# Kernel tuning notes

Measured on AMD Instinct MI355X. Metric: run time of the kernel, lower is better.

## Reference

```python
import jax, jax.numpy as jnp
import numpy as np

B, D_DATA, D_DICT0, N_SAE, D_DICT = 2048, 768, 128, 128, 32


def _kaiming_uniform(key, shape, fan_in):
    # torch.nn.init.kaiming_uniform_ default: bound = sqrt(6 / fan_in) / sqrt(5-gain stuff) ~ use gain=sqrt(2)? match torch default a=sqrt(5) not needed; plain kaiming_uniform_ uses gain=sqrt(2): bound = sqrt(6/fan_in)*? Keep simple: bound = sqrt(6.0/fan_in)
    bound = np.sqrt(6.0 / fan_in)
    return jax.random.uniform(key, shape, jnp.float32, -bound, bound)


def setup_inputs() -> dict:
    key = jax.random.key(0)
    ks = jax.random.split(key, 6)
    x = jax.random.normal(ks[0], (B, D_DATA), jnp.float32)
    # top-level SAE params
    W_enc0 = _kaiming_uniform(ks[1], (D_DATA, D_DICT0), D_DATA)
    b_enc0 = jnp.zeros((D_DICT0,), jnp.float32)
    W_dec0 = _kaiming_uniform(ks[2], (D_DICT0, D_DATA), D_DICT0)
    W_dec0 = W_dec0 / jnp.linalg.norm(W_dec0, axis=-1, keepdims=True)
    b_dec0 = jnp.zeros((D_DATA,), jnp.float32)
    # sublayer (hierarchical) per-expert params
    W_enc1 = _kaiming_uniform(ks[3], (N_SAE, D_DATA, D_DICT), D_DATA)
    b_enc1 = jnp.zeros((N_SAE, D_DICT), jnp.float32)
    W_dec1 = _kaiming_uniform(ks[4], (N_SAE, D_DICT, D_DATA), D_DICT)
    W_dec1 = W_dec1 / jnp.linalg.norm(W_dec1, axis=-1, keepdims=True)
    b_dec1 = jnp.zeros((N_SAE, D_DATA), jnp.float32)
    return {"x": x, "W_enc0": W_enc0, "b_enc0": b_enc0, "W_dec0": W_dec0,
            "b_dec0": b_dec0, "W_enc1": W_enc1, "b_enc1": b_enc1,
            "W_dec1": W_dec1, "b_dec1": b_dec1}


def reference(x, W_enc0, b_enc0, W_dec0, b_dec0, W_enc1, b_enc1, W_dec1, b_dec1):
    # ---- sae_0 (standard SAE; scale/unscale are identity) ----
    acts0 = jax.nn.relu((x - b_dec0) @ W_enc0 + b_enc0)        # [B, D_DICT0]
    x0 = acts0 @ W_dec0 + b_dec0                               # [B, D_DATA]
    # ---- binary gate over experts (n_sae == d_dict0) ----
    gate = (acts0 > 0).astype(x.dtype)                         # [B, N_SAE]
    # ---- sublayer: gather-encode-decode-scatter, expressed densely with a
    # binary mask (gate only selects membership; gate value is not multiplied).
    # Avoid materializing [B, N_SAE, D_DATA] by distributing (x - b_dec1[j]):
    pre = (jnp.einsum('bd,jdk->bjk', x, W_enc1)
           - jnp.einsum('jd,jdk->jk', b_dec1, W_enc1)[None]
           + b_enc1[None])                                     # [B, N_SAE, D_DICT]
    acts1 = jax.nn.relu(pre) * gate[:, :, None]                # zero out ungated
    # scatter_add over experts: sum_j gated (acts1[b,j] @ W_dec1[j] + b_dec1[j])
    dec = jnp.einsum('bjk,jkd->bd', acts1, W_dec1) + gate @ b_dec1  # [B, D_DATA]
    return x0 + dec
```

## Files before the change

### kernel.cpp

```cpp
#include <hip/hip_runtime.h>
#include <hip/hip_bf16.h>
#include <stdint.h>

#define B_SZ   2048
#define DDATA  768
#define NSAE   128
#define NJK    4096
#define KA2    4352
#define SPLITK 4
#define KC2    1088

typedef unsigned short u16;
typedef short bf16x8 __attribute__((ext_vector_type(8)));
typedef float f32x4  __attribute__((ext_vector_type(4)));

static __device__ __forceinline__ u16 f2bf(float f) {
  __hip_bfloat16 h = __float2bfloat16(f);
  return *reinterpret_cast<u16*>(&h);
}

static __device__ __forceinline__ void gload16(const u16* g, u16* l) {
  __builtin_amdgcn_global_load_lds(
      (const __attribute__((address_space(1))) unsigned int*)g,
      (__attribute__((address_space(3))) unsigned int*)l,
      16, 0, 0);
}

__global__ __launch_bounds__(256) void k_front(const float* __restrict__ x,
                                               const float* __restrict__ We0,
                                               const float* __restrict__ be0,
                                               const float* __restrict__ bd0,
                                               const float* __restrict__ We1,
                                               const float* __restrict__ bd1,
                                               const float* __restrict__ be1,
                                               const float* __restrict__ Wd1,
                                               const float* __restrict__ Wd0,
                                               u16* __restrict__ W1T,
                                               float* __restrict__ cvp,
                                               u16* __restrict__ B2T,
                                               u16* __restrict__ xb,
                                               u16* __restrict__ A2) {
  __shared__ float smem[6280];
  const int bid = blockIdx.x, t = threadIdx.x;
  if (bid < 256) {
    const int b0 = bid * 8;
    float* xs  = smem;
    float* xns = smem + 6144;
    float* wns = smem + 6152;
#pragma unroll
    for (int i = 0; i < 6; ++i) {
      int idx = t + i * 256;
      int r = idx / 192, c4 = idx % 192;
      size_t go = (size_t)(b0 + r) * DDATA + c4 * 4;
      float4 v = *(const float4*)&x[go];
      ushort4 o;
      o.x = f2bf(v.x); o.y = f2bf(v.y); o.z = f2bf(v.z); o.w = f2bf(v.w);
      *(ushort4*)&xb[go] = o;
      float4 b4 = *(const float4*)&bd0[c4 * 4];
      v.x -= b4.x; v.y -= b4.y; v.z -= b4.z; v.w -= b4.w;
      *(float4*)&xs[r * DDATA + c4 * 4] = v;
    }
    __syncthreads();
    const int ln = t & 63, rg = t >> 6;
#pragma unroll
    for (int rr = 0; rr < 2; ++rr) {
      int r = rg * 2 + rr;
      float a = 0.f;
#pragma unroll
      for (int q = 0; q < 12; ++q) { float xv = xs[r * DDATA + ln + q * 64]; a += xv * xv; }
#pragma unroll
      for (int sh = 32; sh; sh >>= 1) a += __shfl_xor(a, sh, 64);
      if (ln == 0) xns[r] = a;
    }
    const int j0 = ln * 2;
    const float* xr0 = xs + (rg * 2) * DDATA;
    const float* xr1 = xr0 + DDATA;
    float pa0 = be0[j0], pa1 = be0[j0 + 1];
    float pb0 = pa0, pb1 = pa1;
    float wq0 = 0.f, wq1 = 0.f;
#define GBODY(WQ)                                                         \
    for (int d = 0; d < DDATA; d += 4) {                                  \
      _Pragma("unroll")                                                   \
      for (int dd = 0; dd < 4; ++dd) {                                    \
        float2 w2 = *(const float2*)&We0[(size_t)(d + dd) * 128 + j0];    \
        float a0 = xr0[d + dd], a1 = xr1[d + dd];                         \
        pa0 += a0 * w2.x; pa1 += a0 * w2.y;                               \
        pb0 += a1 * w2.x; pb1 += a1 * w2.y;                               \
        if (WQ) { wq0 += w2.x * w2.x; wq1 += w2.y * w2.y; }               \
      }                                                                   \
    }
    if (rg == 0) { GBODY(1); wns[j0] = sqrtf(wq0); wns[j0 + 1] = sqrtf(wq1); }
    else         { GBODY(0); }
#undef GBODY
    __syncthreads();
    const float sA = sqrtf(xns[rg * 2]), sB = sqrtf(xns[rg * 2 + 1]);
    const float w0 = wns[j0], w1 = wns[j0 + 1];
    const size_t rowA = (size_t)(b0 + rg * 2) * KA2;
    const size_t rowB = rowA + KA2;
    unsigned pka = (unsigned)f2bf(pa0 > 0.f ? pa0 : 0.f) |
                   ((unsigned)f2bf(pa1 > 0.f ? pa1 : 0.f) << 16);
    unsigned gka = (pa0 > 0.f ? 0x3F80u : 0u) | (pa1 > 0.f ? 0x3F800000u : 0u);
    unsigned pkb = (unsigned)f2bf(pb0 > 0.f ? pb0 : 0.f) |
                   ((unsigned)f2bf(pb1 > 0.f ? pb1 : 0.f) << 16);
    unsigned gkb = (pb0 > 0.f ? 0x3F80u : 0u) | (pb1 > 0.f ? 0x3F800000u : 0u);
    *(unsigned*)&A2[rowA + NJK + j0]       = pka;
    *(unsigned*)&A2[rowA + NJK + 128 + j0] = gka;
    *(unsigned*)&A2[rowB + NJK + j0]       = pkb;
    *(unsigned*)&A2[rowB + NJK + 128 + j0] = gkb;
    const float tA0 = 1e-4f * sA * w0, tA1 = 1e-4f * sA * w1;
    const float tB0 = 1e-4f * sB * w0, tB1 = 1e-4f * sB * w1;
#pragma unroll
    for (int c = 0; c < 4; ++c) {
      float pv = c == 0 ? pa0 : c == 1 ? pa1 : c == 2 ? pb0 : pb1;
      float tv = c == 0 ? tA0 : c == 1 ? tA1 : c == 2 ? tB0 : tB1;
      unsigned long long mask = __ballot(fabsf(pv) <= tv);
      const int bb = b0 + rg * 2 + (c >> 1);
      while (mask) {
        int src = (int)__builtin_ctzll(mask);
        mask &= mask - 1;
        int jj = src * 2 + (c & 1);
        double acc = 0.0;
#pragma unroll
        for (int q = 0; q < 12; ++q) {
          int d = ln + q * 64;
          acc += (double)(x[(size_t)bb * DDATA + d] - bd0[d]) *
                 (double)We0[(size_t)d * 128 + jj];
        }
#pragma unroll
        for (int sh = 32; sh; sh >>= 1) acc += __shfl_xor(acc, sh, 64);
        if (ln == src) {
          double pd = acc + (double)be0[jj];
          size_t rw = (size_t)bb * KA2;
          A2[rw + NJK + jj]       = f2bf(pd > 0.0 ? (float)pd : 0.f);
          A2[rw + NJK + 128 + jj] = (pd > 0.0) ? (u16)0x3F80 : (u16)0;
        }
      }
    }
  } else if (bid < 640) {
    const int e = bid - 256;
    const int j = e & 127, seg = e >> 7;
    float* ts  = smem;
    float* bds = smem + 64 * 33;
    float* red = smem + 64 * 33 + 64;
    const int k = t & 31, g = t >> 5;
    float cacc = 0.f;
    for (int db = seg * 4; db < seg * 4 + 4; ++db) {
      const float* src = We1 + (size_t)j * 24576 + db * 2048;
#pragma unroll
      for (int i = 0; i < 8; ++i) {
        int ee = t + i * 256;
        ts[(ee >> 5) * 33 + (ee & 31)] = src[ee];
      }
      if (t < 64) bds[t] = bd1[(size_t)j * DDATA + db * 64 + t];
      __syncthreads();
#pragma unroll
      for (int i = 0; i < 8; ++i) {
        int ee = t + i * 256;
        int kk = ee >> 6, d = ee & 63;
        W1T[(size_t)(j * 32 + kk) * DDATA + db * 64 + d] = f2bf(ts[d * 33 + kk]);
      }
#pragma unroll
      for (int q = 0; q < 8; ++q) {
        int d = g + 8 * q;
        cacc += ts[d * 33 + k] * bds[d];
      }
      __syncthreads();
    }
    red[g * 32 + k] = cacc;
    __syncthreads();
    if (g == 0) {
      float s = 0.f;
#pragma unroll
      for (int q = 0; q < 8; ++q) s += red[q * 32 + k];
      cvp[seg * 4096 + j * 32 + k] = (seg == 0 ? be1[j * 32 + k] : 0.f) - s;
    }
  } else {
    const int e2 = bid - 640;
    const int rb = e2 / 12, dbk = e2 % 12;
    const float* src; int r0, base;
    if (rb < 64)      { src = Wd1; r0 = rb * 64;        base = 0;    }
    else if (rb < 66) { src = Wd0; r0 = (rb - 64) * 64; base = 4096; }
    else              { src = bd1; r0 = (rb - 66) * 64; base = 4224; }
    const int d0 = dbk * 64;
#pragma unroll
    for (int i = 0; i < 16; ++i) {
      int ee = t + i * 256;
      int ri = ee >> 6, di = ee & 63;
      smem[ri * 65 + di] = src[(size_t)(r0 + ri) * DDATA + d0 + di];
    }
    __syncthreads();
#pragma unroll
    for (int i = 0; i < 16; ++i) {
      int ee = t + i * 256;
      int di = ee >> 6, ri = ee & 63;
      B2T[(size_t)(d0 + di) * KA2 + base + r0 + ri] = f2bf(smem[ri * 65 + di]);
    }
  }
}

template<int BM, int BN, int EPI>
__global__ __launch_bounds__(256) void k_gemm(const u16* __restrict__ A,
                                              const u16* __restrict__ Bm,
                                              int K, int Kc,
                                              float* __restrict__ outF,
                                              u16* __restrict__ A2,
                                              const float* __restrict__ cvec) {
  constexpr int WM = BM / 32, WN = BN / 32;
  __shared__ __align__(16) u16 As[BM * 64];
  __shared__ __align__(16) u16 Bs[BN * 64];
  __shared__ u16 gate_s[BM * 4];
  __shared__ float cv_s[BN];
  const int tid = threadIdx.x;
  int bx, by, bz;
  {
    const int h = blockIdx.x;
    if (EPI == 1) {
      const int l = (h & 7) * 64 + (h >> 3);
      const int g2 = l >> 6, w = l & 63;
      by = w >> 2; bx = (g2 << 2) + (w & 3); bz = 0;
    } else {
      const int l = (h & 7) * 96 + (h >> 3);
      bx = l >> 7; const int r2 = l & 127; bz = r2 >> 5; by = r2 & 31;
    }
  }
  const int kbase = bz * Kc;
  const u16* Ab = A  + (size_t)(by * BM) * K;
  const u16* Bb = Bm + (size_t)(bx * BN) * K;
  const int wave = tid >> 6, lane = tid & 63;
  const int wr = wave >> 1, wc = wave & 1;
  const int m0 = wr * (BM / 2), n0 = wc * (BN / 2);
  const int lm = lane & 15, qd = lane >> 4;

  if (EPI == 1) {
    for (int e = tid; e < BM * 4; e += 256) {
      int r = e >> 2, q = e & 3;
      gate_s[e] = A2[(size_t)(by * BM + r) * KA2 + NJK + 128 + bx * 4 + q];
    }
    for (int e = tid; e < BN; e += 256)
      cv_s[e] = cvec[bx * BN + e] + cvec[4096 + bx * BN + e] + cvec[8192 + bx * BN + e];
  }

  f32x4 acc[WM][WN];
  const f32x4 zero = {0.f, 0.f, 0.f, 0.f};
  for (int mi = 0; mi < WM; ++mi)
    for (int ni = 0; ni < WN; ++ni) acc[mi][ni] = zero;

  for (int k0 = kbase; k0 < kbase + Kc; k0 += 64) {
#pragma unroll
    for (int i = 0; i < BM / 32; ++i) {
      int id = tid + 256 * i;
      int row = id >> 3, u = id & 7;
      gload16(Ab + (size_t)row * K + k0 + ((u ^ (row & 7)) * 8), &As[id * 8]);
    }
#pragma unroll
    for (int i = 0; i < BN / 32; ++i) {
      int id = tid + 256 * i;
      int row = id >> 3, u = id & 7;
      gload16(Bb + (size_t)row * K + k0 + ((u ^ (row & 7)) * 8), &Bs[id * 8]);
    }
    __syncthreads();
#pragma unroll
    for (int s = 0; s < 2; ++s) {
      const int swz = ((s << 2) + qd) ^ (lm & 7);
      bf16x8 af[WM], bfv[WN];
#pragma unroll
      for (int mi = 0; mi < WM; ++mi)
        af[mi] = *(const bf16x8*)&As[(m0 + mi * 16 + lm) * 64 + swz * 8];
#pragma unroll
      for (int ni = 0; ni < WN; ++ni)
        bfv[ni] = *(const bf16x8*)&Bs[(n0 + ni * 16 + lm) * 64 + swz * 8];
#pragma unroll
      for (int mi = 0; mi < WM; ++mi)
#pragma unroll
        for (int ni = 0; ni < WN; ++ni)
          acc[mi][ni] = __builtin_amdgcn_mfma_f32_16x16x32_bf16(af[mi], bfv[ni],
                                                                acc[mi][ni], 0, 0, 0);
    }
    __syncthreads();
  }

  const int rb = qd * 4;
#pragma unroll
  for (int mi = 0; mi < WM; ++mi) {
#pragma unroll
    for (int ni = 0; ni < WN; ++ni) {
#pragma unroll
      for (int r = 0; r < 4; ++r) {
        int ml = m0 + mi * 16 + rb + r;
        int nl = n0 + ni * 16 + lm;
        int gm = by * BM + ml;
        int gn = bx * BN + nl;
        float v = acc[mi][ni][r];
        if (EPI == 1) {
          v += cv_s[nl];
          v = v > 0.f ? v : 0.f;
          u16 gbit = gate_s[ml * 4 + (nl >> 5)];
          v = gbit ? v : 0.f;
          float vn = __shfl_xor(v, 1, 64);
          if ((lm & 1) == 0) {
            unsigned pk = (unsigned)f2bf(v) | ((unsigned)f2bf(vn) << 16);
            *(unsigned*)&A2[(size_t)gm * KA2 + gn] = pk;
          }
        } else {
          outF[((size_t)bz * B_SZ + gm) * DDATA + gn] = v;
        }
      }
    }
  }
}

__global__ __launch_bounds__(256) void k_reduce(const float* __restrict__ part,
                                                const float* __restrict__ bias,
                                                float* __restrict__ out) {
  const int N4 = B_SZ * DDATA / 4;
  int i = blockIdx.x * 256 + threadIdx.x;
  const float4* p4 = (const float4*)part;
  float4 s = p4[i];
#pragma unroll
  for (int z = 1; z < SPLITK; ++z) {
    float4 t = p4[i + z * N4];
    s.x += t.x; s.y += t.y; s.z += t.z; s.w += t.w;
  }
  float4 b = ((const float4*)bias)[i % (DDATA / 4)];
  s.x += b.x; s.y += b.y; s.z += b.z; s.w += b.w;
  ((float4*)out)[i] = s;
}

extern "C" void kernel_launch(void* const* d_in, const int* in_sizes, int n_in,
                              void* d_out, int out_size, void* d_ws, size_t ws_size,
                              hipStream_t stream) {
  const float* x   = (const float*)d_in[0];
  const float* We0 = (const float*)d_in[1];
  const float* be0 = (const float*)d_in[2];
  const float* Wd0 = (const float*)d_in[3];
  const float* bd0 = (const float*)d_in[4];
  const float* We1 = (const float*)d_in[5];
  const float* be1 = (const float*)d_in[6];
  const float* Wd1 = (const float*)d_in[7];
  const float* bd1 = (const float*)d_in[8];
  float* out = (float*)d_out;

  uint8_t* ws = (uint8_t*)d_ws;
  size_t off = 0;
  auto carve = [&](size_t bytes) {
    uint8_t* p = ws + off;
    off += (bytes + 255) & ~(size_t)255;
    return p;
  };
  u16*    A2   = (u16*)carve((size_t)B_SZ * KA2 * 2);
  u16*    xb   = (u16*)carve((size_t)B_SZ * DDATA * 2);
  u16*    W1T  = (u16*)carve((size_t)NJK * DDATA * 2);
  u16*    B2T  = (u16*)carve((size_t)DDATA * KA2 * 2);
  float*  cvp  = (float*)carve((size_t)3 * NJK * 4);
  float*  part = (float*)carve((size_t)SPLITK * B_SZ * DDATA * 4);

  k_front <<<1456, 256, 0, stream>>>(x, We0, be0, bd0, We1, bd1, be1, Wd1, Wd0,
                                     W1T, cvp, B2T, xb, A2);
  k_gemm<128, 128, 1><<<512, 256, 0, stream>>>(xb, W1T, DDATA, DDATA,
                                               nullptr, A2, cvp);
  k_gemm<64, 128, 2><<<768, 256, 0, stream>>>(A2, B2T, KA2, KC2,
                                              part, nullptr, nullptr);
  k_reduce<<<1536, 256, 0, stream>>>(part, bd0, out);
}
```

Baseline: 184.2 us.

## Split gate GEMV over d, move B2T transpose into encoder GEMM launch

New measurement: 163.7 us. 1.12x faster.

```diff
diff --git a/kernel.cpp b/kernel.cpp
--- a/kernel.cpp
+++ b/kernel.cpp
@@ -9,6 +9,7 @@
 #define KA2    4352
 #define SPLITK 4
 #define KC2    1088
+#define B2TB   816
 
 typedef unsigned short u16;
 typedef short bf16x8 __attribute__((ext_vector_type(8)));
@@ -33,20 +34,18 @@
                                                const float* __restrict__ We1,
                                                const float* __restrict__ bd1,
                                                const float* __restrict__ be1,
-                                               const float* __restrict__ Wd1,
-                                               const float* __restrict__ Wd0,
                                                u16* __restrict__ W1T,
                                                float* __restrict__ cvp,
-                                               u16* __restrict__ B2T,
                                                u16* __restrict__ xb,
                                                u16* __restrict__ A2) {
-  __shared__ float smem[6280];
+  __shared__ float smem[10760];
   const int bid = blockIdx.x, t = threadIdx.x;
   if (bid < 256) {
     const int b0 = bid * 8;
-    float* xs  = smem;
-    float* xns = smem + 6144;
-    float* wns = smem + 6152;
+    float* xs   = smem;
+    float* part = smem + 6144;
+    float* wqp  = smem + 10240;
+    float* xns  = smem + 10752;
 #pragma unroll
     for (int i = 0; i < 6; ++i) {
       int idx = t + i * 256;
@@ -61,10 +60,10 @@
       *(float4*)&xs[r * DDATA + c4 * 4] = v;
     }
     __syncthreads();
-    const int ln = t & 63, rg = t >> 6;
+    const int ln = t & 63, w = t >> 6;
 #pragma unroll
     for (int rr = 0; rr < 2; ++rr) {
-      int r = rg * 2 + rr;
+      int r = w * 2 + rr;
       float a = 0.f;
 #pragma unroll
       for (int q = 0; q < 12; ++q) { float xv = xs[r * DDATA + ln + q * 64]; a += xv * xv; }
@@ -73,29 +72,46 @@
       if (ln == 0) xns[r] = a;
     }
     const int j0 = ln * 2;
-    const float* xr0 = xs + (rg * 2) * DDATA;
-    const float* xr1 = xr0 + DDATA;
+    float a0[8], a1[8];
+    float wq0 = 0.f, wq1 = 0.f;
+#pragma unroll
+    for (int r = 0; r < 8; ++r) { a0[r] = 0.f; a1[r] = 0.f; }
+    const int dbase = w * 192;
+    for (int d = dbase; d < dbase + 192; d += 4) {
+      float4 xv[8];
+#pragma unroll
+      for (int r = 0; r < 8; ++r) xv[r] = *(const float4*)&xs[r * DDATA + d];
+#pragma unroll
+      for (int dd = 0; dd < 4; ++dd) {
+        float2 w2 = *(const float2*)&We0[(size_t)(d + dd) * 128 + j0];
+#pragma unroll
+        for (int r = 0; r < 8; ++r) {
+          float xr = ((const float*)&xv[r])[dd];
+          a0[r] += xr * w2.x; a1[r] += xr * w2.y;
+        }
+        wq0 += w2.x * w2.x; wq1 += w2.y * w2.y;
+      }
+    }
+#pragma unroll
+    for (int r = 0; r < 8; ++r)
+      *(float2*)&part[(w * 8 + r) * 128 + j0] = make_float2(a0[r], a1[r]);
+    *(float2*)&wqp[w * 128 + j0] = make_float2(wq0, wq1);
+    __syncthreads();
     float pa0 = be0[j0], pa1 = be0[j0 + 1];
     float pb0 = pa0, pb1 = pa1;
-    float wq0 = 0.f, wq1 = 0.f;
-#define GBODY(WQ)                                                         \
-    for (int d = 0; d < DDATA; d += 4) {                                  \
-      _Pragma("unroll")                                                   \
-      for (int dd = 0; dd < 4; ++dd) {                                    \
-        float2 w2 = *(const float2*)&We0[(size_t)(d + dd) * 128 + j0];    \
-        float a0 = xr0[d + dd], a1 = xr1[d + dd];                         \
-        pa0 += a0 * w2.x; pa1 += a0 * w2.y;                               \
-        pb0 += a1 * w2.x; pb1 += a1 * w2.y;                               \
-        if (WQ) { wq0 += w2.x * w2.x; wq1 += w2.y * w2.y; }               \
-      }                                                                   \
-    }
-    if (rg == 0) { GBODY(1); wns[j0] = sqrtf(wq0); wns[j0 + 1] = sqrtf(wq1); }
-    else         { GBODY(0); }
-#undef GBODY
-    __syncthreads();
-    const float sA = sqrtf(xns[rg * 2]), sB = sqrtf(xns[rg * 2 + 1]);
-    const float w0 = wns[j0], w1 = wns[j0 + 1];
-    const size_t rowA = (size_t)(b0 + rg * 2) * KA2;
+    float wn0 = 0.f, wn1 = 0.f;
+#pragma unroll
+    for (int q = 0; q < 4; ++q) {
+      float2 prA = *(const float2*)&part[(q * 8 + 2 * w) * 128 + j0];
+      float2 prB = *(const float2*)&part[(q * 8 + 2 * w + 1) * 128 + j0];
+      pa0 += prA.x; pa1 += prA.y;
+      pb0 += prB.x; pb1 += prB.y;
+      float2 wr2 = *(const float2*)&wqp[q * 128 + j0];
+      wn0 += wr2.x; wn1 += wr2.y;
+    }
+    const float sA = sqrtf(xns[2 * w]), sB = sqrtf(xns[2 * w + 1]);
+    const float w0 = sqrtf(wn0), w1 = sqrtf(wn1);
+    const size_t rowA = (size_t)(b0 + 2 * w) * KA2;
     const size_t rowB = rowA + KA2;
     unsigned pka = (unsigned)f2bf(pa0 > 0.f ? pa0 : 0.f) |
                    ((unsigned)f2bf(pa1 > 0.f ? pa1 : 0.f) << 16);
@@ -114,7 +130,7 @@
       float pv = c == 0 ? pa0 : c == 1 ? pa1 : c == 2 ? pb0 : pb1;
       float tv = c == 0 ? tA0 : c == 1 ? tA1 : c == 2 ? tB0 : tB1;
       unsigned long long mask = __ballot(fabsf(pv) <= tv);
-      const int bb = b0 + rg * 2 + (c >> 1);
+      const int bb = b0 + 2 * w + (c >> 1);
       while (mask) {
         int src = (int)__builtin_ctzll(mask);
         mask &= mask - 1;
@@ -136,7 +152,7 @@
         }
       }
     }
-  } else if (bid < 640) {
+  } else {
     const int e = bid - 256;
     const int j = e & 127, seg = e >> 7;
     float* ts  = smem;
@@ -174,9 +190,31 @@
       for (int q = 0; q < 8; ++q) s += red[q * 32 + k];
       cvp[seg * 4096 + j * 32 + k] = (seg == 0 ? be1[j * 32 + k] : 0.f) - s;
     }
-  } else {
-    const int e2 = bid - 640;
-    const int rb = e2 / 12, dbk = e2 % 12;
+  }
+}
+
+template<int BM, int BN, int EPI, int BK>
+__global__ __launch_bounds__(256) void k_gemm(const u16* __restrict__ A,
+                                              const u16* __restrict__ Bm,
+                                              int K, int Kc,
+                                              float* __restrict__ outF,
+                                              u16* __restrict__ A2,
+                                              const float* __restrict__ cvec,
+                                              const float* __restrict__ Wd1,
+                                              const float* __restrict__ Wd0,
+                                              const float* __restrict__ bd1,
+                                              u16* __restrict__ B2Tp) {
+  constexpr int WM = BM / 32, WN = BN / 32;
+  constexpr int CPR = BK / 8;
+  __shared__ __align__(16) u16 AsBs[(BM + BN) * BK];
+  __shared__ u16 gate_s[BM * 4];
+  __shared__ float cv_s[BN];
+  const int tid = threadIdx.x;
+  const int h = blockIdx.x;
+
+  if (EPI == 1 && h < B2TB) {
+    float* fsm = (float*)&AsBs[0];
+    const int rb = h / 12, dbk = h % 12;
     const float* src; int r0, base;
     if (rb < 64)      { src = Wd1; r0 = rb * 64;        base = 0;    }
     else if (rb < 66) { src = Wd0; r0 = (rb - 64) * 64; base = 4096; }
@@ -184,44 +222,29 @@
     const int d0 = dbk * 64;
 #pragma unroll
     for (int i = 0; i < 16; ++i) {
-      int ee = t + i * 256;
+      int ee = tid + i * 256;
       int ri = ee >> 6, di = ee & 63;
-      smem[ri * 65 + di] = src[(size_t)(r0 + ri) * DDATA + d0 + di];
+      fsm[ri * 65 + di] = src[(size_t)(r0 + ri) * DDATA + d0 + di];
     }
     __syncthreads();
 #pragma unroll
     for (int i = 0; i < 16; ++i) {
-      int ee = t + i * 256;
+      int ee = tid + i * 256;
       int di = ee >> 6, ri = ee & 63;
-      B2T[(size_t)(d0 + di) * KA2 + base + r0 + ri] = f2bf(smem[ri * 65 + di]);
-    }
-  }
-}
-
-template<int BM, int BN, int EPI>
-__global__ __launch_bounds__(256) void k_gemm(const u16* __restrict__ A,
-                                              const u16* __restrict__ Bm,
-                                              int K, int Kc,
-                                              float* __restrict__ outF,
-                                              u16* __restrict__ A2,
-                                              const float* __restrict__ cvec) {
-  constexpr int WM = BM / 32, WN = BN / 32;
-  __shared__ __align__(16) u16 As[BM * 64];
-  __shared__ __align__(16) u16 Bs[BN * 64];
-  __shared__ u16 gate_s[BM * 4];
-  __shared__ float cv_s[BN];
-  const int tid = threadIdx.x;
+      B2Tp[(size_t)(d0 + di) * KA2 + base + r0 + ri] = f2bf(fsm[ri * 65 + di]);
+    }
+    return;
+  }
+
   int bx, by, bz;
-  {
-    const int h = blockIdx.x;
-    if (EPI == 1) {
-      const int l = (h & 7) * 64 + (h >> 3);
-      const int g2 = l >> 6, w = l & 63;
-      by = w >> 2; bx = (g2 << 2) + (w & 3); bz = 0;
-    } else {
-      const int l = (h & 7) * 96 + (h >> 3);
-      bx = l >> 7; const int r2 = l & 127; bz = r2 >> 5; by = r2 & 31;
-    }
+  if (EPI == 1) {
+    const int hg = h - B2TB;
+    const int l = (hg & 7) * 128 + (hg >> 3);
+    const int g2 = l >> 7, w = l & 127;
+    by = w >> 2; bx = (g2 << 2) + (w & 3); bz = 0;
+  } else {
+    const int l = (h & 7) * 96 + (h >> 3);
+    bx = l >> 7; const int r2 = l & 127; bz = r2 >> 5; by = r2 & 31;
   }
   const int kbase = bz * Kc;
   const u16* Ab = A  + (size_t)(by * BM) * K;
@@ -230,6 +253,8 @@
   const int wr = wave >> 1, wc = wave & 1;
   const int m0 = wr * (BM / 2), n0 = wc * (BN / 2);
   const int lm = lane & 15, qd = lane >> 4;
+  u16* As = &AsBs[0];
+  u16* Bs = &AsBs[BM * BK];
 
   if (EPI == 1) {
     for (int e = tid; e < BM * 4; e += 256) {
@@ -245,30 +270,30 @@
   for (int mi = 0; mi < WM; ++mi)
     for (int ni = 0; ni < WN; ++ni) acc[mi][ni] = zero;
 
-  for (int k0 = kbase; k0 < kbase + Kc; k0 += 64) {
-#pragma unroll
-    for (int i = 0; i < BM / 32; ++i) {
+  for (int k0 = kbase; k0 < kbase + Kc; k0 += BK) {
+#pragma unroll
+    for (int i = 0; i < BM * BK / 2048; ++i) {
       int id = tid + 256 * i;
-      int row = id >> 3, u = id & 7;
+      int row = id / CPR, u = id % CPR;
       gload16(Ab + (size_t)row * K + k0 + ((u ^ (row & 7)) * 8), &As[id * 8]);
     }
 #pragma unroll
-    for (int i = 0; i < BN / 32; ++i) {
+    for (int i = 0; i < BN * BK / 2048; ++i) {
       int id = tid + 256 * i;
-      int row = id >> 3, u = id & 7;
+      int row = id / CPR, u = id % CPR;
       gload16(Bb + (size_t)row * K + k0 + ((u ^ (row & 7)) * 8), &Bs[id * 8]);
     }
     __syncthreads();
 #pragma unroll
-    for (int s = 0; s < 2; ++s) {
+    for (int s = 0; s < BK / 32; ++s) {
       const int swz = ((s << 2) + qd) ^ (lm & 7);
       bf16x8 af[WM], bfv[WN];
 #pragma unroll
       for (int mi = 0; mi < WM; ++mi)
-        af[mi] = *(const bf16x8*)&As[(m0 + mi * 16 + lm) * 64 + swz * 8];
+        af[mi] = *(const bf16x8*)&As[(m0 + mi * 16 + lm) * BK + swz * 8];
 #pragma unroll
       for (int ni = 0; ni < WN; ++ni)
-        bfv[ni] = *(const bf16x8*)&Bs[(n0 + ni * 16 + lm) * 64 + swz * 8];
+        bfv[ni] = *(const bf16x8*)&Bs[(n0 + ni * 16 + lm) * BK + swz * 8];
 #pragma unroll
       for (int mi = 0; mi < WM; ++mi)
 #pragma unroll
@@ -354,11 +379,11 @@
   float*  cvp  = (float*)carve((size_t)3 * NJK * 4);
   float*  part = (float*)carve((size_t)SPLITK * B_SZ * DDATA * 4);
 
-  k_front <<<1456, 256, 0, stream>>>(x, We0, be0, bd0, We1, bd1, be1, Wd1, Wd0,
-                                     W1T, cvp, B2T, xb, A2);
-  k_gemm<128, 128, 1><<<512, 256, 0, stream>>>(xb, W1T, DDATA, DDATA,
-                                               nullptr, A2, cvp);
-  k_gemm<64, 128, 2><<<768, 256, 0, stream>>>(A2, B2T, KA2, KC2,
-                                              part, nullptr, nullptr);
+  k_front <<<640, 256, 0, stream>>>(x, We0, be0, bd0, We1, bd1, be1,
+                                    W1T, cvp, xb, A2);
+  k_gemm<64, 128, 1, 128><<<B2TB + 1024, 256, 0, stream>>>(
+      xb, W1T, DDATA, DDATA, nullptr, A2, cvp, Wd1, Wd0, bd1, B2T);
+  k_gemm<64, 128, 2, 64><<<768, 256, 0, stream>>>(
+      A2, B2T, KA2, KC2, part, nullptr, nullptr, nullptr, nullptr, nullptr, nullptr);
   k_reduce<<<1536, 256, 0, stream>>>(part, bd0, out);
 }
```
